# Performance work log

Measured on AMD Instinct MI355X. Metric: run time of the kernel, lower is better.

The kernel has to match this reference:

```python
import jax, jax.numpy as jnp
import numpy as np
import math

B, C, H, W = 16, 1, 1536, 1536


def setup_inputs() -> dict:
    key = jax.random.key(0)
    x = jax.random.normal(key, (B, C, H, W), dtype=jnp.float32)
    return {"inputs": x}


def _remove_nan(v):
    # utils.remove_nan: replace NaNs with zeros
    return jnp.where(jnp.isnan(v), jnp.zeros_like(v), v)


def reference(inputs):
    # Vectorized over batch; tf.map_fn applied axes 1,2 per-sample, which are
    # axes 2,3 (H, W) of the full (B, C, H, W) tensor.
    grad = lambda m, ax: jnp.roll(m, 1, axis=ax) - m
    p = grad(inputs, 2)          # d/dH
    q = grad(inputs, 3)          # d/dW
    r = grad(p, 2)               # d2/dH2
    s = grad(p, 3)               # d2/dHdW
    t = grad(q, 3)               # d2/dW2

    one_pq = 1.0 + p * p + q * q
    # mean curvature
    Hc = _remove_nan(-((1.0 + q * q) * r - 2.0 * p * q * s + (1.0 + p * p) * t)
                     / (2.0 * jnp.sqrt(one_pq ** 3)))
    # gaussian curvature
    Kc = _remove_nan((r * t - s * s) / (one_pq ** 2))

    root = jnp.sqrt(Hc * Hc - Kc)
    k_min = _remove_nan(Hc - root)
    k_max = _remove_nan(Hc + root)

    si = _remove_nan((2.0 / math.pi) * jnp.arctan((k_max + k_min) / (k_max - k_min)))
    return si
```

## Files before the change

### kernel.cpp

```cpp
#include <hip/hip_runtime.h>
#include <cmath>

#define B_ 16
#define H_ 1536
#define W_ 1536

typedef float v4f __attribute__((ext_vector_type(4)));

__global__ __launch_bounds__(384) void ShapeIndex_kernel(
        const float* __restrict__ x, float* __restrict__ out) {
#pragma clang fp contract(off)
    const int h  = blockIdx.x;
    const int b  = blockIdx.y;
    const int w  = threadIdx.x * 4;

    const float* plane = x + (size_t)b * (H_ * W_);
    const int hm1 = (h == 0) ? (H_ - 1) : (h - 1);
    const int hm2 = (h <= 1) ? (h + H_ - 2) : (h - 2);

    const float4 vc = *(const float4*)(plane + h   * W_ + w);
    const float4 v1 = *(const float4*)(plane + hm1 * W_ + w);
    const float4 v2 = *(const float4*)(plane + hm2 * W_ + w);

    const int wm1 = (w == 0) ? (W_ - 1) : (w - 1);
    const int wm2 = (w == 0) ? (W_ - 2) : (w - 2);
    const float L0  = plane[h   * W_ + wm1];
    const float L1  = plane[h   * W_ + wm2];
    const float Lh1 = plane[hm1 * W_ + wm1];

    const v4f xc    = {vc.x, vc.y, vc.z, vc.w};
    const v4f xh1   = {v1.x, v1.y, v1.z, v1.w};
    const v4f xh2   = {v2.x, v2.y, v2.z, v2.w};
    const v4f xw1   = {L0,  vc.x, vc.y, vc.z};
    const v4f xw2   = {L1,  L0,  vc.x, vc.y};
    const v4f xh1w1 = {Lh1, v1.x, v1.y, v1.z};

    const v4f p    = xh1   - xc;
    const v4f q    = xw1   - xc;
    const v4f p_up = xh2   - xh1;
    const v4f p_lf = xh1w1 - xw1;
    const v4f q_lf = xw2   - xw1;
    const v4f r = p_up - p;
    const v4f s = p_lf - p;
    const v4f t = q_lf - q;

    const v4f pp = p * p;
    const v4f qq = q * q;
    const v4f one_pq = (1.0f + pp) + qq;
    const v4f A = ((1.0f + qq) * r - ((2.0f * p) * q) * s) + (1.0f + pp) * t;
    const v4f sq   = one_pq * one_pq;
    const v4f cube = sq * one_pq;
    const v4f numk = r * t - s * s;

    v4f Hc, Kc;
#pragma unroll
    for (int j = 0; j < 4; ++j) {
        Hc[j] = -(A[j] / (2.0f * __builtin_sqrtf(cube[j])));
        Kc[j] = numk[j] / sq[j];
    }

    const v4f disc = Hc * Hc - Kc;
    v4f root;
#pragma unroll
    for (int j = 0; j < 4; ++j) root[j] = __builtin_sqrtf(disc[j]);

    const v4f kmin = Hc - root;
    const v4f kmax = Hc + root;
    const v4f num  = kmax + kmin;
    const v4f den  = kmax - kmin;

    v4f z;
#pragma unroll
    for (int j = 0; j < 4; ++j) z[j] = num[j] * __builtin_amdgcn_rcpf(den[j]);

    v4f u;
    bool big[4];
#pragma unroll
    for (int j = 0; j < 4; ++j) {
        const float az  = __builtin_fabsf(z[j]);
        const float inv = __builtin_amdgcn_rcpf(az);
        big[j] = az > 1.0f;
        u[j]   = big[j] ? inv : az;
    }
    const v4f x2 = u * u;
    const v4f C5 = -0.01172120f, C4 = 0.05265332f, C3 = -0.11643287f,
              C2 = 0.19354346f,  C1 = -0.33262347f, C0 = 0.99997726f;
    v4f pl = __builtin_elementwise_fma(x2, C5, C4);
    pl = __builtin_elementwise_fma(x2, pl, C3);
    pl = __builtin_elementwise_fma(x2, pl, C2);
    pl = __builtin_elementwise_fma(x2, pl, C1);
    pl = __builtin_elementwise_fma(x2, pl, C0);
    const v4f a    = u * pl;
    const v4f asub = 1.57079632679489662f - a;

    v4f rs;
#pragma unroll
    for (int j = 0; j < 4; ++j)
        rs[j] = __builtin_copysignf(big[j] ? asub[j] : a[j], z[j]);
    const v4f siv = 0.63661977236758134f * rs;

    float res[4];
#pragma unroll
    for (int j = 0; j < 4; ++j)
        res[j] = (siv[j] == siv[j]) ? siv[j] : 0.0f;

    *(float4*)(out + (size_t)b * (H_ * W_) + h * W_ + w) =
        make_float4(res[0], res[1], res[2], res[3]);
}

extern "C" void kernel_launch(void* const* d_in, const int* in_sizes, int n_in,
                              void* d_out, int out_size, void* d_ws, size_t ws_size,
                              hipStream_t stream) {
    const float* x = (const float*)d_in[0];
    float* out = (float*)d_out;
    dim3 grid(H_, B_);
    dim3 block(384);
    ShapeIndex_kernel<<<grid, block, 0, stream>>>(x, out);
}
```

Before: 270.4 us.

## Use fast rcp/sqrt with exact fallback near zero discriminant; remap row order

```diff
diff --git a/kernel.cpp b/kernel.cpp
--- a/kernel.cpp
+++ b/kernel.cpp
@@ -10,7 +10,8 @@
 __global__ __launch_bounds__(384) void ShapeIndex_kernel(
         const float* __restrict__ x, float* __restrict__ out) {
 #pragma clang fp contract(off)
-    const int h  = blockIdx.x;
+    const int hraw = blockIdx.x;
+    const int h  = (hraw & 7) * (H_ / 8) + (hraw >> 3);
     const int b  = blockIdx.y;
     const int w  = threadIdx.x * 4;
 
@@ -55,14 +56,39 @@
     v4f Hc, Kc;
 #pragma unroll
     for (int j = 0; j < 4; ++j) {
-        Hc[j] = -(A[j] / (2.0f * __builtin_sqrtf(cube[j])));
-        Kc[j] = numk[j] / sq[j];
+        const float sr = __builtin_amdgcn_sqrtf(cube[j]);
+        Hc[j] = -A[j] * __builtin_amdgcn_rcpf(sr + sr);
+        Kc[j] = numk[j] * __builtin_amdgcn_rcpf(sq[j]);
+    }
+    const v4f HH = Hc * Hc;
+    v4f disc = HH - Kc;
+
+    v4f mag;
+#pragma unroll
+    for (int j = 0; j < 4; ++j) mag[j] = HH[j] + __builtin_fabsf(Kc[j]);
+    const v4f thr = mag * 0x1p-16f;
+    bool need[4];
+    bool any = false;
+#pragma unroll
+    for (int j = 0; j < 4; ++j) {
+        need[j] = __builtin_fabsf(disc[j]) <= thr[j];
+        any |= need[j];
+    }
+    if (__builtin_expect(any, 0)) {
+#pragma unroll
+        for (int j = 0; j < 4; ++j) if (need[j]) {
+            const float se  = __builtin_sqrtf(cube[j]);
+            const float hce = -(A[j] / (2.0f * se));
+            const float kce = numk[j] / sq[j];
+            Hc[j]   = hce;
+            Kc[j]   = kce;
+            disc[j] = hce * hce - kce;
+        }
     }
 
-    const v4f disc = Hc * Hc - Kc;
     v4f root;
 #pragma unroll
-    for (int j = 0; j < 4; ++j) root[j] = __builtin_sqrtf(disc[j]);
+    for (int j = 0; j < 4; ++j) root[j] = __builtin_amdgcn_sqrtf(disc[j]);
 
     const v4f kmin = Hc - root;
     const v4f kmax = Hc + root;
```

New measurement: 256.6 us. 5.1% less time.
